# Performance work log

Measured on AMD Instinct MI355X. Metric: run time of the kernel, lower is better.

## Reference

```python
import jax, jax.numpy as jnp
import numpy as np

HOPS = 3  # max_hops; C has HOPS+1 embedding tables


def setup_inputs() -> dict:
    key = jax.random.key(0)
    k1, k2 = jax.random.split(key)
    # story: [memory_len, batch, token_size]
    story = jax.random.randint(k1, (2048, 64, 4), 0, 50000, dtype=jnp.int64)
    # stacked embedding tables C_0..C_3: [hop+1, vocab, embed_dim], N(0, 0.1)
    C = 0.1 * jax.random.normal(k2, (HOPS + 1, 50000, 128), dtype=jnp.float32)
    return {"story": story, "C": C}


def reference(story, C):
    # story: [M, B, T] -> [B, M, T]
    story = jnp.transpose(story, (1, 0, 2))
    B, M, T = story.shape
    D = C.shape[-1]
    # padding_idx=0 semantics: embedding of token 0 is zero (fwd and bwd)
    pad_mask = (story != 0).astype(C.dtype)[..., None]  # [B, M, T, 1]

    u = jnp.zeros((B, D), dtype=C.dtype)
    for hop in range(HOPS):
        # gather + mask + sum over token dim -> memory keys m_A: [B, M, D]
        m_A = jnp.sum(C[hop][story] * pad_mask, axis=2)
        # attention scores over memory slots, softmax along M
        prob = jax.nn.softmax(jnp.einsum('bmd,bd->bm', m_A, u), axis=1)
        # memory values m_C from next-hop table: [B, M, D]
        m_C = jnp.sum(C[hop + 1][story] * pad_mask, axis=2)
        o_k = jnp.einsum('bm,bmd->bd', prob, m_C)
        u = u + o_k
    return u
```

## Files before the change

kernel.cpp:

```cpp
#include <hip/hip_runtime.h>

#define MM 2048
#define BB 64
#define TT 4
#define DD 128
#define VV 50000
#define VPAD 50176
#define NPART 392

typedef float f4v __attribute__((ext_vector_type(4)));
typedef short s8v __attribute__((ext_vector_type(8)));

__device__ __forceinline__ unsigned short f2bf(float f) {
    unsigned int u = __float_as_uint(f);
    u = u + 0x7FFFu + ((u >> 16) & 1u);
    return (unsigned short)(u >> 16);
}

__global__ void k_init(float4* __restrict__ p) {
    p[blockIdx.x * 256 + threadIdx.x] = make_float4(0.f, 0.f, 0.f, 0.f);
}

__global__ __launch_bounds__(256, 4) void k_gemm_p(const float* __restrict__ Ch,
                                                   const float* __restrict__ u,
                                                   float* __restrict__ P) {
    __shared__ short lds[128 * 136];
    const int t = threadIdx.x;
    const int v0 = blockIdx.x * 64;

#pragma unroll
    for (int i = 0; i < 16; ++i) {
        const int G = i * 256 + t;
        const int row = G >> 5;
        const int c4 = G & 31;
        float4 val;
        if (row < 64) {
            const int v = v0 + row;
            val = (v < VV) ? *(const float4*)(Ch + (size_t)v * DD + c4 * 4)
                           : make_float4(0.f, 0.f, 0.f, 0.f);
        } else {
            val = *(const float4*)(u + (size_t)(row - 64) * DD + c4 * 4);
        }
        const unsigned int lo = ((unsigned int)f2bf(val.y) << 16) | f2bf(val.x);
        const unsigned int hi = ((unsigned int)f2bf(val.w) << 16) | f2bf(val.z);
        *(uint2*)(lds + row * 136 + c4 * 4) = make_uint2(lo, hi);
    }
    __syncthreads();

    const int l = t & 63;
    const int w = t >> 6;
    const int quad = l >> 4;
    const int n16 = l & 15;

    const int arow = (16 * w + n16) * 136;
    const int brow0 = (64 + 0 * 16 + n16) * 136;
    const int brow1 = (64 + 1 * 16 + n16) * 136;
    const int brow2 = (64 + 2 * 16 + n16) * 136;
    const int brow3 = (64 + 3 * 16 + n16) * 136;

    f4v ac0 = {0.f, 0.f, 0.f, 0.f}, ac1 = ac0, ac2 = ac0, ac3 = ac0;

#pragma unroll
    for (int s = 0; s < 4; ++s) {
        const int ko = s * 32 + quad * 8;
        const s8v av = *(const s8v*)(lds + arow + ko);
        const s8v b0 = *(const s8v*)(lds + brow0 + ko);
        const s8v b1 = *(const s8v*)(lds + brow1 + ko);
        const s8v b2 = *(const s8v*)(lds + brow2 + ko);
        const s8v b3 = *(const s8v*)(lds + brow3 + ko);
        ac0 = __builtin_amdgcn_mfma_f32_16x16x32_bf16(av, b0, ac0, 0, 0, 0);
        ac1 = __builtin_amdgcn_mfma_f32_16x16x32_bf16(av, b1, ac1, 0, 0, 0);
        ac2 = __builtin_amdgcn_mfma_f32_16x16x32_bf16(av, b2, ac2, 0, 0, 0);
        ac3 = __builtin_amdgcn_mfma_f32_16x16x32_bf16(av, b3, ac3, 0, 0, 0);
    }

    const int vbase = v0 + 16 * w + quad * 4;
#pragma unroll
    for (int r = 0; r < 4; ++r) {
        float* __restrict__ Pr = P + (size_t)(vbase + r) * 64 + n16;
        Pr[0]  = ac0[r];
        Pr[16] = ac1[r];
        Pr[32] = ac2[r];
        Pr[48] = ac3[r];
    }
}

__global__ __launch_bounds__(512) void k_attn(const int* __restrict__ st,
                                              const float* __restrict__ P,
                                              float* __restrict__ W) {
    const int b = blockIdx.x;
    const int tid = threadIdx.x;
    __shared__ float redmax[8];
    __shared__ float redsum[8];

    const int4 tk0 = *(const int4*)(st + ((size_t)(tid + 0)    * 64 + b) * 4);
    const int4 tk1 = *(const int4*)(st + ((size_t)(tid + 512)  * 64 + b) * 4);
    const int4 tk2 = *(const int4*)(st + ((size_t)(tid + 1024) * 64 + b) * 4);
    const int4 tk3 = *(const int4*)(st + ((size_t)(tid + 1536) * 64 + b) * 4);

    float v0 = 0.f, v1 = 0.f, v2 = 0.f, v3 = 0.f;
    if (tk0.x) v0 += P[(size_t)tk0.x * 64 + b];
    if (tk0.y) v0 += P[(size_t)tk0.y * 64 + b];
    if (tk0.z) v0 += P[(size_t)tk0.z * 64 + b];
    if (tk0.w) v0 += P[(size_t)tk0.w * 64 + b];
    if (tk1.x) v1 += P[(size_t)tk1.x * 64 + b];
    if (tk1.y) v1 += P[(size_t)tk1.y * 64 + b];
    if (tk1.z) v1 += P[(size_t)tk1.z * 64 + b];
    if (tk1.w) v1 += P[(size_t)tk1.w * 64 + b];
    if (tk2.x) v2 += P[(size_t)tk2.x * 64 + b];
    if (tk2.y) v2 += P[(size_t)tk2.y * 64 + b];
    if (tk2.z) v2 += P[(size_t)tk2.z * 64 + b];
    if (tk2.w) v2 += P[(size_t)tk2.w * 64 + b];
    if (tk3.x) v3 += P[(size_t)tk3.x * 64 + b];
    if (tk3.y) v3 += P[(size_t)tk3.y * 64 + b];
    if (tk3.z) v3 += P[(size_t)tk3.z * 64 + b];
    if (tk3.w) v3 += P[(size_t)tk3.w * 64 + b];

    float mx = fmaxf(fmaxf(v0, v1), fmaxf(v2, v3));
#pragma unroll
    for (int off = 32; off; off >>= 1) mx = fmaxf(mx, __shfl_xor(mx, off, 64));
    if ((tid & 63) == 0) redmax[tid >> 6] = mx;
    __syncthreads();
    float gmax = redmax[0];
#pragma unroll
    for (int i = 1; i < 8; ++i) gmax = fmaxf(gmax, redmax[i]);

    v0 = __expf(v0 - gmax); v1 = __expf(v1 - gmax);
    v2 = __expf(v2 - gmax); v3 = __expf(v3 - gmax);
    float sum = (v0 + v1) + (v2 + v3);
#pragma unroll
    for (int off = 32; off; off >>= 1) sum += __shfl_xor(sum, off, 64);
    if ((tid & 63) == 0) redsum[tid >> 6] = sum;
    __syncthreads();
    float tot = redsum[0];
#pragma unroll
    for (int i = 1; i < 8; ++i) tot += redsum[i];
    const float inv = 1.f / tot;

    v0 *= inv; v1 *= inv; v2 *= inv; v3 *= inv;

    if (tk0.x) atomicAdd(W + (size_t)tk0.x * 64 + b, v0);
    if (tk0.y) atomicAdd(W + (size_t)tk0.y * 64 + b, v0);
    if (tk0.z) atomicAdd(W + (size_t)tk0.z * 64 + b, v0);
    if (tk0.w) atomicAdd(W + (size_t)tk0.w * 64 + b, v0);
    if (tk1.x) atomicAdd(W + (size_t)tk1.x * 64 + b, v1);
    if (tk1.y) atomicAdd(W + (size_t)tk1.y * 64 + b, v1);
    if (tk1.z) atomicAdd(W + (size_t)tk1.z * 64 + b, v1);
    if (tk1.w) atomicAdd(W + (size_t)tk1.w * 64 + b, v1);
    if (tk2.x) atomicAdd(W + (size_t)tk2.x * 64 + b, v2);
    if (tk2.y) atomicAdd(W + (size_t)tk2.y * 64 + b, v2);
    if (tk2.z) atomicAdd(W + (size_t)tk2.z * 64 + b, v2);
    if (tk2.w) atomicAdd(W + (size_t)tk2.w * 64 + b, v2);
    if (tk3.x) atomicAdd(W + (size_t)tk3.x * 64 + b, v3);
    if (tk3.y) atomicAdd(W + (size_t)tk3.y * 64 + b, v3);
    if (tk3.z) atomicAdd(W + (size_t)tk3.z * 64 + b, v3);
    if (tk3.w) atomicAdd(W + (size_t)tk3.w * 64 + b, v3);
}

__global__ __launch_bounds__(256, 3) void k_gemm_o(const float* __restrict__ C2,
                                                   float* __restrict__ W,
                                                   float* __restrict__ upart,
                                                   const int rezero) {
    __shared__ float Wl[64 * 68];
    __shared__ float Cl[64 * 136];
    const int t = threadIdx.x;
    const int g = t >> 7;
    const int b0 = ((t >> 4) & 7) * 8;
    const int d0 = (t & 15) * 8;
    const int vb = blockIdx.x * 128;

    f4v a0l = {0.f, 0.f, 0.f, 0.f}, a0h = a0l, a1l = a0l, a1h = a0l;
    f4v a2l = a0l, a2h = a0l, a3l = a0l, a3h = a0l;
    f4v a4l = a0l, a4h = a0l, a5l = a0l, a5h = a0l;
    f4v a6l = a0l, a6h = a0l, a7l = a0l, a7h = a0l;

    for (int cc = 0; cc < 2; ++cc) {
        const int vc = vb + cc * 64;
#pragma unroll
        for (int i = 0; i < 4; ++i) {
            const int G = i * 256 + t;
            const int row = G >> 4, c4 = G & 15;
            float* wp = W + (size_t)(vc + row) * 64 + c4 * 4;
            const float4 val = *(const float4*)wp;
            *(float4*)&Wl[row * 68 + c4 * 4] = val;
            if (rezero) *(float4*)wp = make_float4(0.f, 0.f, 0.f, 0.f);
        }
#pragma unroll
        for (int i = 0; i < 8; ++i) {
            const int G = i * 256 + t;
            const int row = G >> 5, c4 = G & 31;
            const int v = vc + row;
            float4 val = (v < VV) ? *(const float4*)(C2 + (size_t)v * DD + c4 * 4)
                                  : make_float4(0.f, 0.f, 0.f, 0.f);
            *(float4*)&Cl[row * 136 + c4 * 4] = val;
        }
        __syncthreads();

#define FMA_ROW(al, ah, wc)            \
    al += wc * cA; ah += wc * cB;

#pragma unroll
        for (int j = 0; j < 32; ++j) {
            const int kk = g * 32 + j;
            const f4v wA = *(const f4v*)&Wl[kk * 68 + b0];
            const f4v wB = *(const f4v*)&Wl[kk * 68 + b0 + 4];
            const f4v cA = *(const f4v*)&Cl[kk * 136 + d0];
            const f4v cB = *(const f4v*)&Cl[kk * 136 + d0 + 4];
            FMA_ROW(a0l, a0h, wA[0]) FMA_ROW(a1l, a1h, wA[1])
            FMA_ROW(a2l, a2h, wA[2]) FMA_ROW(a3l, a3h, wA[3])
            FMA_ROW(a4l, a4h, wB[0]) FMA_ROW(a5l, a5h, wB[1])
            FMA_ROW(a6l, a6h, wB[2]) FMA_ROW(a7l, a7h, wB[3])
        }
#undef FMA_ROW
        __syncthreads();
    }

    if (g == 1) {
#define STL(i, al, ah)                                   \
        *(f4v*)&Cl[(b0 + i) * 136 + d0] = al;            \
        *(f4v*)&Cl[(b0 + i) * 136 + d0 + 4] = ah;
        STL(0, a0l, a0h) STL(1, a1l, a1h) STL(2, a2l, a2h) STL(3, a3l, a3h)
        STL(4, a4l, a4h) STL(5, a5l, a5h) STL(6, a6l, a6h) STL(7, a7l, a7h)
#undef STL
    }
    __syncthreads();
    if (g == 0) {
        float* __restrict__ up = upart + (size_t)blockIdx.x * (BB * DD);
#define STG(i, al, ah) {                                             \
        const f4v xl = al + *(const f4v*)&Cl[(b0 + i) * 136 + d0];   \
        const f4v xh = ah + *(const f4v*)&Cl[(b0 + i) * 136 + d0 + 4]; \
        *(f4v*)(up + (b0 + i) * DD + d0) = xl;                       \
        *(f4v*)(up + (b0 + i) * DD + d0 + 4) = xh; }
        STG(0, a0l, a0h) STG(1, a1l, a1h) STG(2, a2l, a2h) STG(3, a3l, a3h)
        STG(4, a4l, a4h) STG(5, a5l, a5h) STG(6, a6l, a6h) STG(7, a7l, a7h)
#undef STG
    }
}

__global__ __launch_bounds__(256) void k_reduce_u(const float* __restrict__ up,
                                                  float* __restrict__ u) {
    const int jc = blockIdx.x & 31;
    const int kc = blockIdx.x >> 5;
    const int j = jc * 256 + threadIdx.x;
    const float* __restrict__ p = up + (size_t)kc * 49 * (BB * DD) + j;
    float s = 0.f;
#pragma unroll 7
    for (int k = 0; k < 49; ++k) s += p[(size_t)k * (BB * DD)];
    atomicAdd(u + j, s);
}

__global__ void k_copy(const float* __restrict__ u, float* __restrict__ out) {
    const int i = blockIdx.x * 256 + threadIdx.x;
    out[i] = u[i];
}

extern "C" void kernel_launch(void* const* d_in, const int* in_sizes, int n_in,
                              void* d_out, int out_size, void* d_ws, size_t ws_size,
                              hipStream_t stream) {
    const int* st = (const int*)d_in[0];
    const float* C = (const float*)d_in[1];

    float* u  = (float*)d_ws;
    float* W  = u + BB * DD;
    float* P  = W + (size_t)VPAD * BB;
    float* up = P + (size_t)VPAD * BB;

    k_init<<<(BB * DD + VPAD * BB) / 1024, 256, 0, stream>>>((float4*)u);

    for (int hop = 0; hop < 3; ++hop) {
        const float* Ch  = C + (size_t)hop * VV * DD;
        const float* Ch1 = C + (size_t)(hop + 1) * VV * DD;

        k_gemm_p<<<VPAD / 64, 256, 0, stream>>>(Ch, u, P);
        k_attn<<<BB, 512, 0, stream>>>(st, P, W);
        k_gemm_o<<<VPAD / 128, 256, 0, stream>>>(Ch1, W, up,
                                                 hop < 2 ? 1 : 0);
        k_reduce_u<<<256, 256, 0, stream>>>(up, u);
    }

    k_copy<<<(BB * DD) / 256, 256, 0, stream>>>(u, (float*)d_out);
}
```

Before: 377.0 us.

## Drop max-subtracted softmax and defer normalization to parallelize attention kernel

Measured after the change: 383.7 us. About the same (+1.8%).

```diff
diff --git a/kernel.cpp b/kernel.cpp
--- a/kernel.cpp
+++ b/kernel.cpp
@@ -23,10 +23,13 @@
 
 __global__ __launch_bounds__(256, 4) void k_gemm_p(const float* __restrict__ Ch,
                                                    const float* __restrict__ u,
-                                                   float* __restrict__ P) {
+                                                   float* __restrict__ P,
+                                                   float* __restrict__ Z) {
     __shared__ short lds[128 * 136];
     const int t = threadIdx.x;
     const int v0 = blockIdx.x * 64;
+
+    if (blockIdx.x == 0 && t < 64) Z[t] = 0.f;
 
 #pragma unroll
     for (int i = 0; i < 16; ++i) {
@@ -85,76 +88,32 @@
     }
 }
 
-__global__ __launch_bounds__(512) void k_attn(const int* __restrict__ st,
-                                              const float* __restrict__ P,
-                                              float* __restrict__ W) {
-    const int b = blockIdx.x;
+__global__ __launch_bounds__(256) void k_attn2(const int* __restrict__ st,
+                                               const float* __restrict__ P,
+                                               float* __restrict__ W,
+                                               float* __restrict__ Z) {
+    __shared__ float eb[256];
     const int tid = threadIdx.x;
-    __shared__ float redmax[8];
-    __shared__ float redsum[8];
-
-    const int4 tk0 = *(const int4*)(st + ((size_t)(tid + 0)    * 64 + b) * 4);
-    const int4 tk1 = *(const int4*)(st + ((size_t)(tid + 512)  * 64 + b) * 4);
-    const int4 tk2 = *(const int4*)(st + ((size_t)(tid + 1024) * 64 + b) * 4);
-    const int4 tk3 = *(const int4*)(st + ((size_t)(tid + 1536) * 64 + b) * 4);
-
-    float v0 = 0.f, v1 = 0.f, v2 = 0.f, v3 = 0.f;
-    if (tk0.x) v0 += P[(size_t)tk0.x * 64 + b];
-    if (tk0.y) v0 += P[(size_t)tk0.y * 64 + b];
-    if (tk0.z) v0 += P[(size_t)tk0.z * 64 + b];
-    if (tk0.w) v0 += P[(size_t)tk0.w * 64 + b];
-    if (tk1.x) v1 += P[(size_t)tk1.x * 64 + b];
-    if (tk1.y) v1 += P[(size_t)tk1.y * 64 + b];
-    if (tk1.z) v1 += P[(size_t)tk1.z * 64 + b];
-    if (tk1.w) v1 += P[(size_t)tk1.w * 64 + b];
-    if (tk2.x) v2 += P[(size_t)tk2.x * 64 + b];
-    if (tk2.y) v2 += P[(size_t)tk2.y * 64 + b];
-    if (tk2.z) v2 += P[(size_t)tk2.z * 64 + b];
-    if (tk2.w) v2 += P[(size_t)tk2.w * 64 + b];
-    if (tk3.x) v3 += P[(size_t)tk3.x * 64 + b];
-    if (tk3.y) v3 += P[(size_t)tk3.y * 64 + b];
-    if (tk3.z) v3 += P[(size_t)tk3.z * 64 + b];
-    if (tk3.w) v3 += P[(size_t)tk3.w * 64 + b];
-
-    float mx = fmaxf(fmaxf(v0, v1), fmaxf(v2, v3));
-#pragma unroll
-    for (int off = 32; off; off >>= 1) mx = fmaxf(mx, __shfl_xor(mx, off, 64));
-    if ((tid & 63) == 0) redmax[tid >> 6] = mx;
+    const int g = blockIdx.x * 256 + tid;
+    const int b = g & 63;
+
+    const int4 tk = *(const int4*)(st + (size_t)g * 4);
+    float s = 0.f;
+    if (tk.x) s += P[(size_t)tk.x * 64 + b];
+    if (tk.y) s += P[(size_t)tk.y * 64 + b];
+    if (tk.z) s += P[(size_t)tk.z * 64 + b];
+    if (tk.w) s += P[(size_t)tk.w * 64 + b];
+    const float e = __expf(s);
+    eb[tid] = e;
+
+    if (tk.x) atomicAdd(W + (size_t)tk.x * 64 + b, e);
+    if (tk.y) atomicAdd(W + (size_t)tk.y * 64 + b, e);
+    if (tk.z) atomicAdd(W + (size_t)tk.z * 64 + b, e);
+    if (tk.w) atomicAdd(W + (size_t)tk.w * 64 + b, e);
+
     __syncthreads();
-    float gmax = redmax[0];
-#pragma unroll
-    for (int i = 1; i < 8; ++i) gmax = fmaxf(gmax, redmax[i]);
-
-    v0 = __expf(v0 - gmax); v1 = __expf(v1 - gmax);
-    v2 = __expf(v2 - gmax); v3 = __expf(v3 - gmax);
-    float sum = (v0 + v1) + (v2 + v3);
-#pragma unroll
-    for (int off = 32; off; off >>= 1) sum += __shfl_xor(sum, off, 64);
-    if ((tid & 63) == 0) redsum[tid >> 6] = sum;
-    __syncthreads();
-    float tot = redsum[0];
-#pragma unroll
-    for (int i = 1; i < 8; ++i) tot += redsum[i];
-    const float inv = 1.f / tot;
-
-    v0 *= inv; v1 *= inv; v2 *= inv; v3 *= inv;
-
-    if (tk0.x) atomicAdd(W + (size_t)tk0.x * 64 + b, v0);
-    if (tk0.y) atomicAdd(W + (size_t)tk0.y * 64 + b, v0);
-    if (tk0.z) atomicAdd(W + (size_t)tk0.z * 64 + b, v0);
-    if (tk0.w) atomicAdd(W + (size_t)tk0.w * 64 + b, v0);
-    if (tk1.x) atomicAdd(W + (size_t)tk1.x * 64 + b, v1);
-    if (tk1.y) atomicAdd(W + (size_t)tk1.y * 64 + b, v1);
-    if (tk1.z) atomicAdd(W + (size_t)tk1.z * 64 + b, v1);
-    if (tk1.w) atomicAdd(W + (size_t)tk1.w * 64 + b, v1);
-    if (tk2.x) atomicAdd(W + (size_t)tk2.x * 64 + b, v2);
-    if (tk2.y) atomicAdd(W + (size_t)tk2.y * 64 + b, v2);
-    if (tk2.z) atomicAdd(W + (size_t)tk2.z * 64 + b, v2);
-    if (tk2.w) atomicAdd(W + (size_t)tk2.w * 64 + b, v2);
-    if (tk3.x) atomicAdd(W + (size_t)tk3.x * 64 + b, v3);
-    if (tk3.y) atomicAdd(W + (size_t)tk3.y * 64 + b, v3);
-    if (tk3.z) atomicAdd(W + (size_t)tk3.z * 64 + b, v3);
-    if (tk3.w) atomicAdd(W + (size_t)tk3.w * 64 + b, v3);
+    if (tid < 64)
+        atomicAdd(Z + tid, (eb[tid] + eb[tid + 64]) + (eb[tid + 128] + eb[tid + 192]));
 }
 
 __global__ __launch_bounds__(256, 3) void k_gemm_o(const float* __restrict__ C2,
@@ -238,6 +197,7 @@
 }
 
 __global__ __launch_bounds__(256) void k_reduce_u(const float* __restrict__ up,
+                                                  const float* __restrict__ Z,
                                                   float* __restrict__ u) {
     const int jc = blockIdx.x & 31;
     const int kc = blockIdx.x >> 5;
@@ -246,7 +206,8 @@
     float s = 0.f;
 #pragma unroll 7
     for (int k = 0; k < 49; ++k) s += p[(size_t)k * (BB * DD)];
-    atomicAdd(u + j, s);
+    const float rz = 1.f / Z[j >> 7];
+    atomicAdd(u + j, s * rz);
 }
 
 __global__ void k_copy(const float* __restrict__ u, float* __restrict__ out) {
@@ -264,6 +225,7 @@
     float* W  = u + BB * DD;
     float* P  = W + (size_t)VPAD * BB;
     float* up = P + (size_t)VPAD * BB;
+    float* Z  = up + (size_t)NPART * BB * DD;
 
     k_init<<<(BB * DD + VPAD * BB) / 1024, 256, 0, stream>>>((float4*)u);
 
@@ -271,11 +233,11 @@
         const float* Ch  = C + (size_t)hop * VV * DD;
         const float* Ch1 = C + (size_t)(hop + 1) * VV * DD;
 
-        k_gemm_p<<<VPAD / 64, 256, 0, stream>>>(Ch, u, P);
-        k_attn<<<BB, 512, 0, stream>>>(st, P, W);
+        k_gemm_p<<<VPAD / 64, 256, 0, stream>>>(Ch, u, P, Z);
+        k_attn2<<<(MM * BB) / 256, 256, 0, stream>>>(st, P, W, Z);
         k_gemm_o<<<VPAD / 128, 256, 0, stream>>>(Ch1, W, up,
                                                  hop < 2 ? 1 : 0);
-        k_reduce_u<<<256, 256, 0, stream>>>(up, u);
+        k_reduce_u<<<256, 256, 0, stream>>>(up, Z, u);
     }
 
     k_copy<<<(BB * DD) / 256, 256, 0, stream>>>(u, (float*)d_out);
```

## Specialize first hop as uniform scatter, drop softmax max pass, fuse final copy

Applied to the files above, without the earlier changes.

Measured after the change: 388.4 us. +3.0%, slower.

```diff
diff --git a/kernel.cpp b/kernel.cpp
--- a/kernel.cpp
+++ b/kernel.cpp
@@ -19,6 +19,18 @@
 
 __global__ void k_init(float4* __restrict__ p) {
     p[blockIdx.x * 256 + threadIdx.x] = make_float4(0.f, 0.f, 0.f, 0.f);
+}
+
+__global__ __launch_bounds__(256) void k_scatter0(const int* __restrict__ st,
+                                                  float* __restrict__ W) {
+    const int g = blockIdx.x * 256 + threadIdx.x;
+    const int b = g & 63;
+    const float p = 1.0f / (float)MM;
+    const int4 tk = *(const int4*)(st + (size_t)g * 4);
+    if (tk.x) atomicAdd(W + (size_t)tk.x * 64 + b, p);
+    if (tk.y) atomicAdd(W + (size_t)tk.y * 64 + b, p);
+    if (tk.z) atomicAdd(W + (size_t)tk.z * 64 + b, p);
+    if (tk.w) atomicAdd(W + (size_t)tk.w * 64 + b, p);
 }
 
 __global__ __launch_bounds__(256, 4) void k_gemm_p(const float* __restrict__ Ch,
@@ -90,7 +102,6 @@
                                               float* __restrict__ W) {
     const int b = blockIdx.x;
     const int tid = threadIdx.x;
-    __shared__ float redmax[8];
     __shared__ float redsum[8];
 
     const int4 tk0 = *(const int4*)(st + ((size_t)(tid + 0)    * 64 + b) * 4);
@@ -116,17 +127,7 @@
     if (tk3.z) v3 += P[(size_t)tk3.z * 64 + b];
     if (tk3.w) v3 += P[(size_t)tk3.w * 64 + b];
 
-    float mx = fmaxf(fmaxf(v0, v1), fmaxf(v2, v3));
-#pragma unroll
-    for (int off = 32; off; off >>= 1) mx = fmaxf(mx, __shfl_xor(mx, off, 64));
-    if ((tid & 63) == 0) redmax[tid >> 6] = mx;
-    __syncthreads();
-    float gmax = redmax[0];
-#pragma unroll
-    for (int i = 1; i < 8; ++i) gmax = fmaxf(gmax, redmax[i]);
-
-    v0 = __expf(v0 - gmax); v1 = __expf(v1 - gmax);
-    v2 = __expf(v2 - gmax); v3 = __expf(v3 - gmax);
+    v0 = __expf(v0); v1 = __expf(v1); v2 = __expf(v2); v3 = __expf(v3);
     float sum = (v0 + v1) + (v2 + v3);
 #pragma unroll
     for (int off = 32; off; off >>= 1) sum += __shfl_xor(sum, off, 64);
@@ -237,21 +238,15 @@
     }
 }
 
-__global__ __launch_bounds__(256) void k_reduce_u(const float* __restrict__ up,
-                                                  float* __restrict__ u) {
-    const int jc = blockIdx.x & 31;
-    const int kc = blockIdx.x >> 5;
-    const int j = jc * 256 + threadIdx.x;
-    const float* __restrict__ p = up + (size_t)kc * 49 * (BB * DD) + j;
+__global__ __launch_bounds__(256) void k_reduce(const float* __restrict__ up,
+                                                const float* __restrict__ u,
+                                                float* __restrict__ dst) {
+    const int j = blockIdx.x * 256 + threadIdx.x;
+    const float* __restrict__ p = up + j;
     float s = 0.f;
-#pragma unroll 7
-    for (int k = 0; k < 49; ++k) s += p[(size_t)k * (BB * DD)];
-    atomicAdd(u + j, s);
-}
-
-__global__ void k_copy(const float* __restrict__ u, float* __restrict__ out) {
-    const int i = blockIdx.x * 256 + threadIdx.x;
-    out[i] = u[i];
+#pragma unroll 8
+    for (int k = 0; k < NPART; ++k) s += p[(size_t)k * (BB * DD)];
+    dst[j] = u[j] + s;
 }
 
 extern "C" void kernel_launch(void* const* d_in, const int* in_sizes, int n_in,
@@ -267,16 +262,18 @@
 
     k_init<<<(BB * DD + VPAD * BB) / 1024, 256, 0, stream>>>((float4*)u);
 
-    for (int hop = 0; hop < 3; ++hop) {
+    k_scatter0<<<(MM * BB) / 256, 256, 0, stream>>>(st, W);
+    k_gemm_o<<<VPAD / 128, 256, 0, stream>>>(C + (size_t)1 * VV * DD, W, up, 1);
+    k_reduce<<<32, 256, 0, stream>>>(up, u, u);
+
+    for (int hop = 1; hop < 3; ++hop) {
         const float* Ch  = C + (size_t)hop * VV * DD;
-        const float* Ch1 = C + (size_t)(hop + 1) * VV * DD;
+        const float* Ch1 = Ch + (size_t)VV * DD;
+        const int last = (hop == 2);
 
         k_gemm_p<<<VPAD / 64, 256, 0, stream>>>(Ch, u, P);
         k_attn<<<BB, 512, 0, stream>>>(st, P, W);
-        k_gemm_o<<<VPAD / 128, 256, 0, stream>>>(Ch1, W, up,
-                                                 hop < 2 ? 1 : 0);
-        k_reduce_u<<<256, 256, 0, stream>>>(up, u);
-    }
-
-    k_copy<<<(BB * DD) / 256, 256, 0, stream>>>(u, (float*)d_out);
-}
+        k_gemm_o<<<VPAD / 128, 256, 0, stream>>>(Ch1, W, up, !last);
+        k_reduce<<<32, 256, 0, stream>>>(up, u, last ? (float*)d_out : u);
+    }
+}
```
